# Kernel tuning notes

Hardware: AMD Instinct MI355X
Metric: run time of the kernel (lower is better)

## Reference

```python
import jax, jax.numpy as jnp
import numpy as np

N = 8192   # number of points
C = 64     # feature channels (in_channels == out_channels in PointTrans_Layer)
K = 16     # KNNGraph(k=16)


def mlp2(h, w1, b1, gamma, beta, w2, b2):
    # PyG MLP(num_layers=2): Linear -> BatchNorm(eval: affine) -> ReLU -> Linear
    h = h @ w1 + b1
    h = gamma * h + beta          # BN in eval mode with running mean 0 / var 1
    h = jax.nn.relu(h)
    return h @ w2 + b2


def knn_indices(pos, k):
    # pairwise squared distances, self excluded (KNNGraph loop=False)
    sq = jnp.sum(pos * pos, axis=-1)                      # [N]
    d = sq[:, None] + sq[None, :] - 2.0 * (pos @ pos.T)   # [N, N]
    n = pos.shape[0]
    d = d.at[jnp.arange(n), jnp.arange(n)].set(jnp.inf)
    _, idx = jax.lax.top_k(-d, k)                         # [N, k] nearest neighbors
    return idx


def setup_inputs() -> dict:
    key = jax.random.key(0)
    ks = jax.random.split(key, 20)
    s = 1.0 / np.sqrt(C)
    inp = {
        "x": jax.random.normal(ks[0], (N, C), jnp.float32),
        "pos": jax.random.uniform(ks[1], (N, 3), jnp.float32) * 10.0,
        # PointTransformerConv linears
        "w_src": jax.random.normal(ks[2], (C, C), jnp.float32) * s,   # lin_src (no bias)
        "w_dst": jax.random.normal(ks[3], (C, C), jnp.float32) * s,   # lin_dst (no bias)
        "w_lin": jax.random.normal(ks[4], (C, C), jnp.float32) * s,   # lin (value)
        "b_lin": jnp.zeros((C,), jnp.float32),
        # pos_nn: MLP(3 -> C -> C)
        "p1w": jax.random.normal(ks[5], (3, C), jnp.float32) * (1.0 / np.sqrt(3)),
        "p1b": jnp.zeros((C,), jnp.float32),
        "p1g": jnp.ones((C,), jnp.float32),
        "p1bt": jnp.zeros((C,), jnp.float32),
        "p2w": jax.random.normal(ks[6], (C, C), jnp.float32) * s,
        "p2b": jnp.zeros((C,), jnp.float32),
        # attn_nn: MLP(C -> C -> C)
        "a1w": jax.random.normal(ks[7], (C, C), jnp.float32) * s,
        "a1b": jnp.zeros((C,), jnp.float32),
        "a1g": jnp.ones((C,), jnp.float32),
        "a1bt": jnp.zeros((C,), jnp.float32),
        "a2w": jax.random.normal(ks[8], (C, C), jnp.float32) * s,
        "a2b": jnp.zeros((C,), jnp.float32),
        # linear_up
        "uw": jax.random.normal(ks[9], (C, C), jnp.float32) * s,
        "ub": jnp.zeros((C,), jnp.float32),
    }
    return inp


def reference(x, pos, w_src, w_dst, w_lin, b_lin,
              p1w, p1b, p1g, p1bt, p2w, p2b,
              a1w, a1b, a1g, a1bt, a2w, a2b, uw, ub):
    idx = knn_indices(pos, K)                       # [N, K] neighbor (source) ids
    a_dst = x @ w_dst                               # alpha_i   [N, C]
    a_src = x @ w_src                               # alpha_j   [N, C]
    v = x @ w_lin + b_lin                           # values    [N, C]

    rel = pos[:, None, :] - pos[idx]                # pos_i - pos_j  [N, K, 3]
    delta = mlp2(rel, p1w, p1b, p1g, p1bt, p2w, p2b)            # [N, K, C]
    alpha = a_dst[:, None, :] - a_src[idx] + delta              # [N, K, C]
    alpha = mlp2(alpha, a1w, a1b, a1g, a1bt, a2w, a2b)          # [N, K, C]
    w = jax.nn.softmax(alpha, axis=1)               # softmax over incoming edges
    out = jnp.sum(w * (v[idx] + delta), axis=1)     # [N, C]

    out = out @ uw + ub                             # linear_up
    return out + x                                  # residual
```

## Files before the change

kernel.cpp:

```cpp
#include <hip/hip_runtime.h>
#include <math.h>

#define N 8192
#define C 64
#define K 16
#define NB 8
#define QB 8
#define LNODES 8
#define HS 72

typedef unsigned long long u64;
typedef unsigned int u32;

typedef float  f32x4v  __attribute__((ext_vector_type(4)));
typedef __bf16 bf16x8  __attribute__((ext_vector_type(8)));

__device__ __forceinline__ unsigned short bfr(float f) {
    u32 u = __float_as_uint(f);
    return (unsigned short)((u + 0x7fffu + ((u >> 16) & 1u)) >> 16);
}

__global__ __launch_bounds__(256) void prep_all(const float* __restrict__ pos,
                                                float4* __restrict__ pos4,
                                                const float* __restrict__ p2w,
                                                const float* __restrict__ a1w,
                                                const float* __restrict__ a2w,
                                                unsigned short* __restrict__ wT) {
    const int id = blockIdx.x * 256 + threadIdx.x;
    if (id < N) {
        const float px = pos[3*id], py = pos[3*id+1], pz = pos[3*id+2];
        pos4[id] = make_float4(px, py, pz, fmaf(px, px, fmaf(py, py, pz * pz)));
    } else {
        const int t = id - N;
        if (t < 3 * C * C) {
            const int m = t >> 12, r = t & (C*C - 1);
            const int e = r >> 6, c = r & 63;
            const float* w = (m == 0) ? p2w : (m == 1) ? a1w : a2w;
            wT[m * C * HS + c * HS + e] = bfr(w[r]);
        }
    }
}

__global__ __launch_bounds__(192) void lin3_kernel(const float* __restrict__ x,
    const float* __restrict__ w_src, const float* __restrict__ w_dst,
    const float* __restrict__ w_lin, const float* __restrict__ b_lin,
    float* __restrict__ a_dst, float* __restrict__ a_src, float* __restrict__ v) {
    __shared__ float xr[LNODES][C];
    const int n0  = blockIdx.x * LNODES;
    const int tid = threadIdx.x;
    const int cc  = tid & 63;
    const int m   = tid >> 6;

    const float* w = (m == 0) ? w_dst : (m == 1) ? w_src : w_lin;
    float wreg[C];
    #pragma unroll
    for (int k = 0; k < C; ++k) wreg[k] = w[k*C + cc];

    for (int t = tid; t < LNODES*C; t += 192) xr[t >> 6][t & 63] = x[n0*C + t];
    __syncthreads();

    const float binit = (m == 2) ? b_lin[cc] : 0.0f;
    float* o = (m == 0) ? a_dst : (m == 1) ? a_src : v;
    for (int nn = 0; nn < LNODES; ++nn) {
        float acc = binit;
        const float4* xv = (const float4*)xr[nn];
        #pragma unroll
        for (int k4 = 0; k4 < 16; ++k4) {
            const float4 xx = xv[k4];
            acc = fmaf(xx.x, wreg[4*k4+0], acc);
            acc = fmaf(xx.y, wreg[4*k4+1], acc);
            acc = fmaf(xx.z, wreg[4*k4+2], acc);
            acc = fmaf(xx.w, wreg[4*k4+3], acc);
        }
        o[(n0 + nn)*C + cc] = acc;
    }
}

__device__ __forceinline__ void mm16x64(const unsigned short* Hb, const unsigned short* wT,
                                        int c0, int sg, f32x4v acc[4]) {
    const bf16x8 a0 = *reinterpret_cast<const bf16x8*>(Hb + c0*HS + sg*8);
    const bf16x8 a1 = *reinterpret_cast<const bf16x8*>(Hb + c0*HS + 32 + sg*8);
    #pragma unroll
    for (int q = 0; q < 4; ++q) {
        const unsigned short* wr = wT + (q*16 + c0)*HS + sg*8;
        const bf16x8 b0 = *reinterpret_cast<const bf16x8*>(wr);
        const bf16x8 b1 = *reinterpret_cast<const bf16x8*>(wr + 32);
        acc[q] = __builtin_amdgcn_mfma_f32_16x16x32_bf16(a0, b0, acc[q], 0, 0, 0);
        acc[q] = __builtin_amdgcn_mfma_f32_16x16x32_bf16(a1, b1, acc[q], 0, 0, 0);
    }
}

struct __align__(16) KnnSh {
    float          smin[QB][512];
    double         s_d[QB][96];
    double         s_fd[QB][K];
    int            s_buf[QB][96];
    int            s_fi[QB][K];
    unsigned short s_tl[QB][64];
    int            s_cnt[QB];
    int            s_tlc[QB];
};
struct __align__(16) EdgeSh {
    unsigned short sWT[3 * C * HS];
    unsigned short sHb[NB * K * HS];
    float4         sMisc4[NB * 16];
};

__global__ __launch_bounds__(512, 6) void knn_edge_kernel(
    const float4* __restrict__ pos4,
    const float* __restrict__ x,
    const float* __restrict__ a_dst, const float* __restrict__ a_src, const float* __restrict__ v,
    const unsigned short* __restrict__ wTg,
    const float* __restrict__ p1w, const float* __restrict__ p1b,
    const float* __restrict__ p1g, const float* __restrict__ p1bt,
    const float* __restrict__ p2b,
    const float* __restrict__ a1b, const float* __restrict__ a1g, const float* __restrict__ a1bt,
    const float* __restrict__ a2b,
    const float* __restrict__ uw, const float* __restrict__ ub,
    float* __restrict__ out) {

    __shared__ union __align__(16) ShU { KnnSh k; EdgeSh e; } sh;
    __shared__ int sIdxL[NB * K];

    const int tid  = threadIdx.x;
    const int w    = tid >> 6;
    const int lane = tid & 63;
    const int i0   = blockIdx.x * QB;

    if (tid < QB) { sh.k.s_cnt[tid] = 0; sh.k.s_tlc[tid] = 0; }

    float qx[QB], qy[QB], qz[QB];
    #pragma unroll
    for (int q = 0; q < QB; ++q) {
        const float4 p = pos4[i0 + q];
        qx[q] = p.x; qy[q] = p.y; qz[q] = p.z;
    }

    {
        float mn[QB];
        #pragma unroll
        for (int q = 0; q < QB; ++q) mn[q] = INFINITY;
        #pragma unroll 4
        for (int s = 0; s < 16; ++s) {
            const int j = (s << 9) + tid;
            const float4 pj = pos4[j];
            #pragma unroll
            for (int q = 0; q < QB; ++q) {
                const float dot = fmaf(qx[q], pj.x, fmaf(qy[q], pj.y, qz[q] * pj.z));
                const float pr  = fmaf(-2.0f, dot, pj.w);
                mn[q] = fminf(mn[q], pr);
            }
        }
        #pragma unroll
        for (int q = 0; q < QB; ++q) sh.k.smin[q][tid] = mn[q];
    }
    __syncthreads();

    float thw;
    {
        float vv[8];
        #pragma unroll
        for (int k = 0; k < 8; ++k) vv[k] = sh.k.smin[w][lane + 64*k];
        float ml = fminf(fminf(fminf(vv[0], vv[1]), fminf(vv[2], vv[3])),
                         fminf(fminf(vv[4], vv[5]), fminf(vv[6], vv[7])));
        float cur = ml, T = 0.0f;
        for (int r = 0; r < K + 1; ++r) {
            float m = cur;
            #pragma unroll
            for (int off = 32; off; off >>= 1) m = fminf(m, __shfl_xor(m, off, 64));
            T = m;
            cur = (cur == m) ? INFINITY : cur;
        }
        thw = T + 1e-3f + 4e-6f * fabsf(T);
        #pragma unroll
        for (int k = 0; k < 8; ++k) {
            if (vv[k] <= thw) {
                const int slot = atomicAdd(&sh.k.s_tlc[w], 1);
                if (slot < 64) sh.k.s_tl[w][slot] = (unsigned short)(lane + 64*k);
            }
        }
    }

    {
        const int lc_raw = sh.k.s_tlc[w];
        const int lc = lc_raw < 64 ? lc_raw : 64;
        const float qwx = qx[w], qwy = qy[w], qwz = qz[w];
        for (int p = lane; p < lc * 16; p += 64) {
            const int t = sh.k.s_tl[w][p >> 4];
            const int s = p & 15;
            const int j = (s << 9) + t;
            const float4 pj = pos4[j];
            const float dot = fmaf(qwx, pj.x, fmaf(qwy, pj.y, qwz * pj.z));
            const float pr  = fmaf(-2.0f, dot, pj.w);
            if (pr <= thw) {
                const int slot = atomicAdd(&sh.k.s_cnt[w], 1);
                if (slot < 96) sh.k.s_buf[w][slot] = j;
            }
        }
    }

    {
        const int q  = w;
        const int iq = i0 + q;
        const int cno = sh.k.s_cnt[q];
        if (cno <= 96 && sh.k.s_tlc[q] <= 64) {
            const int cn = cno;
            const double dqx = (double)qx[q], dqy = (double)qy[q], dqz = (double)qz[q];
            for (int sl = lane; sl < cn; sl += 64) {
                const int jj = sh.k.s_buf[q][sl];
                const float4 pj = pos4[jj];
                const double dx = dqx - (double)pj.x;
                const double dy = dqy - (double)pj.y;
                const double dz = dqz - (double)pj.z;
                sh.k.s_d[q][sl] = dx*dx + dy*dy + dz*dz;
            }
            for (int sl = lane; sl < cn; sl += 64) {
                const int jj = sh.k.s_buf[q][sl];
                if (jj == iq) continue;
                const double dj = sh.k.s_d[q][sl];
                int r = 0;
                for (int e = 0; e < cn; ++e) {
                    const double de = sh.k.s_d[q][e];
                    const int    je = sh.k.s_buf[q][e];
                    r += (de < dj || (de == dj && je < jj)) ? 1 : 0;
                }
                const int selfb = (dj > 0.0 || (dj == 0.0 && iq < jj)) ? 1 : 0;
                const int rr = r - selfb;
                if (rr < K) sIdxL[q*K + rr] = jj;
            }
        } else {
            if (lane == 0) {
                for (int kk = 0; kk < K; ++kk) { sh.k.s_fd[w][kk] = 1e300; sh.k.s_fi[w][kk] = 0x7fffffff; }
                const double dqx = (double)qx[q], dqy = (double)qy[q], dqz = (double)qz[q];
                for (int j = 0; j < N; ++j) {
                    if (j == iq) continue;
                    const float4 pj = pos4[j];
                    const double dx = dqx - (double)pj.x;
                    const double dy = dqy - (double)pj.y;
                    const double dz = dqz - (double)pj.z;
                    const double dd = dx*dx + dy*dy + dz*dz;
                    if (dd < sh.k.s_fd[w][K-1] || (dd == sh.k.s_fd[w][K-1] && j < sh.k.s_fi[w][K-1])) {
                        int p = K - 1;
                        while (p > 0 && (dd < sh.k.s_fd[w][p-1] || (dd == sh.k.s_fd[w][p-1] && j < sh.k.s_fi[w][p-1]))) {
                            sh.k.s_fd[w][p] = sh.k.s_fd[w][p-1]; sh.k.s_fi[w][p] = sh.k.s_fi[w][p-1]; --p;
                        }
                        sh.k.s_fd[w][p] = dd; sh.k.s_fi[w][p] = j;
                    }
                }
                for (int kk = 0; kk < K; ++kk) sIdxL[w*K + kk] = sh.k.s_fi[w][kk];
            }
        }
    }
    __syncthreads();

    const int c0 = tid & 15;
    const int sg = (tid >> 4) & 3;
    const int n  = i0 + w;

    unsigned short* Hlb = sh.e.sHb + w * (K * HS);
    float4*         Ml4 = sh.e.sMisc4 + w * 16;
    int*            Il  = sIdxL + w * K;

    {
        const float4* s4 = (const float4*)wTg;
        float4* d4 = (float4*)sh.e.sWT;
        #pragma unroll
        for (int q = 0; q < 4; ++q) {
            const int e = tid + q*512;
            if (e < 1728) d4[e] = s4[e];
        }
    }
    if (lane < K) {
        const int j = Il[lane];
        const float4 pn = pos4[n];
        const float4 pj = pos4[j];
        Ml4[lane] = make_float4(pn.x - pj.x, pn.y - pj.y, pn.z - pj.z, 0.0f);
    }
    __syncthreads();

    int c4[4];
    #pragma unroll
    for (int q = 0; q < 4; ++q) c4[q] = q*16 + c0;

    {
        float W0[4], W1[4], W2[4], B_[4], G_[4], BT[4];
        #pragma unroll
        for (int q = 0; q < 4; ++q) {
            const int cc = c4[q];
            W0[q] = p1w[cc]; W1[q] = p1w[C + cc]; W2[q] = p1w[2*C + cc];
            B_[q] = p1b[cc]; G_[q] = p1g[cc];     BT[q] = p1bt[cc];
        }
        #pragma unroll
        for (int r = 0; r < 4; ++r) {
            const float4 rr = Ml4[sg*4 + r];
            #pragma unroll
            for (int q = 0; q < 4; ++q) {
                float t = fmaf(rr.x, W0[q], fmaf(rr.y, W1[q], fmaf(rr.z, W2[q], B_[q])));
                t = fmaxf(fmaf(G_[q], t, BT[q]), 0.0f);
                Hlb[(sg*4 + r)*HS + c4[q]] = bfr(t);
            }
        }
    }

    f32x4v acc[4], del[4];
    #pragma unroll
    for (int q = 0; q < 4; ++q) { const float b_ = p2b[c4[q]]; acc[q] = (f32x4v){b_, b_, b_, b_}; }
    mm16x64(Hlb, sh.e.sWT, c0, sg, acc);
    #pragma unroll
    for (int q = 0; q < 4; ++q) del[q] = acc[q];

    int jr[4];
    #pragma unroll
    for (int r = 0; r < 4; ++r) jr[r] = Il[sg*4 + r];
    float adstv[4];
    #pragma unroll
    for (int q = 0; q < 4; ++q) adstv[q] = a_dst[n*C + c4[q]];

    #pragma unroll
    for (int r = 0; r < 4; ++r) {
        #pragma unroll
        for (int q = 0; q < 4; ++q) {
            const float t = adstv[q] - a_src[jr[r]*C + c4[q]] + acc[q][r];
            Hlb[(sg*4 + r)*HS + c4[q]] = bfr(t);
        }
    }

    #pragma unroll
    for (int q = 0; q < 4; ++q) { const float b_ = a1b[c4[q]]; acc[q] = (f32x4v){b_, b_, b_, b_}; }
    mm16x64(Hlb, sh.e.sWT + C*HS, c0, sg, acc);
    #pragma unroll
    for (int q = 0; q < 4; ++q) {
        const float g_ = a1g[c4[q]], bt_ = a1bt[c4[q]];
        #pragma unroll
        for (int r = 0; r < 4; ++r) {
            const float h2 = fmaxf(fmaf(g_, acc[q][r], bt_), 0.0f);
            Hlb[(sg*4 + r)*HS + c4[q]] = bfr(h2);
        }
    }

    #pragma unroll
    for (int q = 0; q < 4; ++q) { const float b_ = a2b[c4[q]]; acc[q] = (f32x4v){b_, b_, b_, b_}; }
    mm16x64(Hlb, sh.e.sWT + 2*C*HS, c0, sg, acc);

    float o_[4];
    #pragma unroll
    for (int q = 0; q < 4; ++q) {
        float vgq[4];
        #pragma unroll
        for (int r = 0; r < 4; ++r) vgq[r] = v[jr[r]*C + c4[q]];
        float lm = fmaxf(fmaxf(acc[q][0], acc[q][1]), fmaxf(acc[q][2], acc[q][3]));
        lm = fmaxf(lm, __shfl_xor(lm, 16, 64));
        lm = fmaxf(lm, __shfl_xor(lm, 32, 64));
        float ls = 0.0f, lo = 0.0f;
        #pragma unroll
        for (int r = 0; r < 4; ++r) {
            const float e_ = __expf(acc[q][r] - lm);
            ls += e_;
            lo = fmaf(e_, vgq[r] + del[q][r], lo);
        }
        ls += __shfl_xor(ls, 16, 64); ls += __shfl_xor(ls, 32, 64);
        lo += __shfl_xor(lo, 16, 64); lo += __shfl_xor(lo, 32, 64);
        o_[q] = lo / ls;
    }
    float* Mlf = (float*)Ml4;
    if (sg == 0) {
        #pragma unroll
        for (int q = 0; q < 4; ++q) Mlf[c4[q]] = o_[q];
    }

    float facc = ub[lane] + x[n*C + lane];
    #pragma unroll 4
    for (int e4 = 0; e4 < 16; ++e4) {
        const float4 g4 = Ml4[e4];
        facc = fmaf(g4.x, uw[(e4*4+0)*C + lane], facc);
        facc = fmaf(g4.y, uw[(e4*4+1)*C + lane], facc);
        facc = fmaf(g4.z, uw[(e4*4+2)*C + lane], facc);
        facc = fmaf(g4.w, uw[(e4*4+3)*C + lane], facc);
    }
    out[n*C + lane] = facc;
}

extern "C" void kernel_launch(void* const* d_in, const int* in_sizes, int n_in,
                              void* d_out, int out_size, void* d_ws, size_t ws_size,
                              hipStream_t stream) {
    const float* x     = (const float*)d_in[0];
    const float* pos   = (const float*)d_in[1];
    const float* w_src = (const float*)d_in[2];
    const float* w_dst = (const float*)d_in[3];
    const float* w_lin = (const float*)d_in[4];
    const float* b_lin = (const float*)d_in[5];
    const float* p1w   = (const float*)d_in[6];
    const float* p1b   = (const float*)d_in[7];
    const float* p1g   = (const float*)d_in[8];
    const float* p1bt  = (const float*)d_in[9];
    const float* p2w   = (const float*)d_in[10];
    const float* p2b   = (const float*)d_in[11];
    const float* a1w   = (const float*)d_in[12];
    const float* a1b   = (const float*)d_in[13];
    const float* a1g   = (const float*)d_in[14];
    const float* a1bt  = (const float*)d_in[15];
    const float* a2w   = (const float*)d_in[16];
    const float* a2b   = (const float*)d_in[17];
    const float* uw    = (const float*)d_in[18];
    const float* ub    = (const float*)d_in[19];
    float* out = (float*)d_out;

    char* ws    = (char*)d_ws;
    float*  adst = (float*)ws;
    float*  asrc = adst + (size_t)N*C;
    float*  vv   = asrc + (size_t)N*C;
    float4* pos4 = (float4*)(vv + (size_t)N*C);
    unsigned short* wTg = (unsigned short*)(pos4 + N);

    prep_all<<<(N + 3*C*C + 255)/256, 256, 0, stream>>>(pos, pos4, p2w, a1w, a2w, wTg);
    lin3_kernel<<<N/LNODES, 192, 0, stream>>>(x, w_src, w_dst, w_lin, b_lin, adst, asrc, vv);
    knn_edge_kernel<<<N/QB, 512, 0, stream>>>(pos4, x, adst, asrc, vv, wTg,
        p1w, p1b, p1g, p1bt, p2b, a1b, a1g, a1bt, a2b, uw, ub, out);
}
```

Baseline: 63.75 us.

## Stream MLP weights through one shared buffer and cheapen KNN threshold search

The three 64x64 bf16 weight matrices now pass through a single shared-memory buffer that is reloaded before each matmul stage, with extra block barriers around each reload. This cuts LDS use and raises the launch-bounds occupancy hint from 6 to 8 waves. The KNN threshold search keeps the two smallest candidates per lane, so the wave-wide min reduction runs 9 rounds instead of 17. Candidate buffers grow to absorb the looser threshold, at the cost of more barriers, repeated global weight loads, and more candidates to rank.

```diff
diff --git a/kernel.cpp b/kernel.cpp
--- a/kernel.cpp
+++ b/kernel.cpp
@@ -92,21 +92,21 @@
 
 struct __align__(16) KnnSh {
     float          smin[QB][512];
-    double         s_d[QB][96];
+    double         s_d[QB][128];
     double         s_fd[QB][K];
-    int            s_buf[QB][96];
+    int            s_buf[QB][128];
     int            s_fi[QB][K];
-    unsigned short s_tl[QB][64];
+    unsigned short s_tl[QB][96];
     int            s_cnt[QB];
     int            s_tlc[QB];
 };
 struct __align__(16) EdgeSh {
-    unsigned short sWT[3 * C * HS];
+    unsigned short wbuf[C * HS];
     unsigned short sHb[NB * K * HS];
     float4         sMisc4[NB * 16];
 };
 
-__global__ __launch_bounds__(512, 6) void knn_edge_kernel(
+__global__ __launch_bounds__(512, 8) void knn_edge_kernel(
     const float4* __restrict__ pos4,
     const float* __restrict__ x,
     const float* __restrict__ a_dst, const float* __restrict__ a_src, const float* __restrict__ v,
@@ -161,10 +161,16 @@
         float vv[8];
         #pragma unroll
         for (int k = 0; k < 8; ++k) vv[k] = sh.k.smin[w][lane + 64*k];
-        float ml = fminf(fminf(fminf(vv[0], vv[1]), fminf(vv[2], vv[3])),
-                         fminf(fminf(vv[4], vv[5]), fminf(vv[6], vv[7])));
-        float cur = ml, T = 0.0f;
-        for (int r = 0; r < K + 1; ++r) {
+        float m1 = INFINITY, m2 = INFINITY;
+        #pragma unroll
+        for (int k = 0; k < 8; ++k) {
+            const float val = vv[k];
+            const bool lt = val < m1;
+            m2 = lt ? m1 : fminf(m2, val);
+            m1 = lt ? val : m1;
+        }
+        float cur = m2, T = 0.0f;
+        for (int r = 0; r < 9; ++r) {
             float m = cur;
             #pragma unroll
             for (int off = 32; off; off >>= 1) m = fminf(m, __shfl_xor(m, off, 64));
@@ -176,14 +182,14 @@
         for (int k = 0; k < 8; ++k) {
             if (vv[k] <= thw) {
                 const int slot = atomicAdd(&sh.k.s_tlc[w], 1);
-                if (slot < 64) sh.k.s_tl[w][slot] = (unsigned short)(lane + 64*k);
+                if (slot < 96) sh.k.s_tl[w][slot] = (unsigned short)(lane + 64*k);
             }
         }
     }
 
     {
         const int lc_raw = sh.k.s_tlc[w];
-        const int lc = lc_raw < 64 ? lc_raw : 64;
+        const int lc = lc_raw < 96 ? lc_raw : 96;
         const float qwx = qx[w], qwy = qy[w], qwz = qz[w];
         for (int p = lane; p < lc * 16; p += 64) {
             const int t = sh.k.s_tl[w][p >> 4];
@@ -194,7 +200,7 @@
             const float pr  = fmaf(-2.0f, dot, pj.w);
             if (pr <= thw) {
                 const int slot = atomicAdd(&sh.k.s_cnt[w], 1);
-                if (slot < 96) sh.k.s_buf[w][slot] = j;
+                if (slot < 128) sh.k.s_buf[w][slot] = j;
             }
         }
     }
@@ -203,7 +209,7 @@
         const int q  = w;
         const int iq = i0 + q;
         const int cno = sh.k.s_cnt[q];
-        if (cno <= 96 && sh.k.s_tlc[q] <= 64) {
+        if (cno <= 128 && sh.k.s_tlc[q] <= 96) {
             const int cn = cno;
             const double dqx = (double)qx[q], dqy = (double)qy[q], dqz = (double)qz[q];
             for (int sl = lane; sl < cn; sl += 64) {
@@ -263,12 +269,9 @@
 
     {
         const float4* s4 = (const float4*)wTg;
-        float4* d4 = (float4*)sh.e.sWT;
-        #pragma unroll
-        for (int q = 0; q < 4; ++q) {
-            const int e = tid + q*512;
-            if (e < 1728) d4[e] = s4[e];
-        }
+        float4* d4 = (float4*)sh.e.wbuf;
+        d4[tid] = s4[tid];
+        if (tid < 64) d4[tid + 512] = s4[tid + 512];
     }
     if (lane < K) {
         const int j = Il[lane];
@@ -276,7 +279,6 @@
         const float4 pj = pos4[j];
         Ml4[lane] = make_float4(pn.x - pj.x, pn.y - pj.y, pn.z - pj.z, 0.0f);
     }
-    __syncthreads();
 
     int c4[4];
     #pragma unroll
@@ -301,11 +303,12 @@
             }
         }
     }
+    __syncthreads();
 
     f32x4v acc[4], del[4];
     #pragma unroll
     for (int q = 0; q < 4; ++q) { const float b_ = p2b[c4[q]]; acc[q] = (f32x4v){b_, b_, b_, b_}; }
-    mm16x64(Hlb, sh.e.sWT, c0, sg, acc);
+    mm16x64(Hlb, sh.e.wbuf, c0, sg, acc);
     #pragma unroll
     for (int q = 0; q < 4; ++q) del[q] = acc[q];
 
@@ -324,10 +327,18 @@
             Hlb[(sg*4 + r)*HS + c4[q]] = bfr(t);
         }
     }
+    __syncthreads();
+    {
+        const float4* s4 = (const float4*)(wTg) + 576;
+        float4* d4 = (float4*)sh.e.wbuf;
+        d4[tid] = s4[tid];
+        if (tid < 64) d4[tid + 512] = s4[tid + 512];
+    }
+    __syncthreads();
 
     #pragma unroll
     for (int q = 0; q < 4; ++q) { const float b_ = a1b[c4[q]]; acc[q] = (f32x4v){b_, b_, b_, b_}; }
-    mm16x64(Hlb, sh.e.sWT + C*HS, c0, sg, acc);
+    mm16x64(Hlb, sh.e.wbuf, c0, sg, acc);
     #pragma unroll
     for (int q = 0; q < 4; ++q) {
         const float g_ = a1g[c4[q]], bt_ = a1bt[c4[q]];
@@ -337,10 +348,18 @@
             Hlb[(sg*4 + r)*HS + c4[q]] = bfr(h2);
         }
     }
+    __syncthreads();
+    {
+        const float4* s4 = (const float4*)(wTg) + 1152;
+        float4* d4 = (float4*)sh.e.wbuf;
+        d4[tid] = s4[tid];
+        if (tid < 64) d4[tid + 512] = s4[tid + 512];
+    }
+    __syncthreads();
 
     #pragma unroll
     for (int q = 0; q < 4; ++q) { const float b_ = a2b[c4[q]]; acc[q] = (f32x4v){b_, b_, b_, b_}; }
-    mm16x64(Hlb, sh.e.sWT + 2*C*HS, c0, sg, acc);
+    mm16x64(Hlb, sh.e.wbuf, c0, sg, acc);
 
     float o_[4];
     #pragma unroll
```

New measurement: 73.84 us. +15.8%, slower.
